# Kernel tuning notes

Hardware: AMD Instinct MI355X
Metric: run time of the kernel (lower is better)

Reference implementation:

```python
import jax, jax.numpy as jnp
import numpy as np

B, S, D_IN, D_OUT, RANK = 4, 2048, 4096, 4096, 16
ALPHA = 16
SCALING = ALPHA / RANK  # 1.0


def setup_inputs() -> dict:
    key = jax.random.key(0)
    k_x, k_q, k_b, k_a, k_bb = jax.random.split(key, 5)
    x = jax.random.normal(k_x, (B, S, D_IN), dtype=jnp.float32)
    # int4 symmetric quantized weight values in [-8, 7], stored as int32
    qweight = jax.random.randint(k_q, (D_OUT, D_IN), -8, 8, dtype=jnp.int32)
    # per-tensor scale (abs_max / 7 in the original); a plausible small value
    scales = jnp.array([0.01], dtype=jnp.float32)
    bias = jax.random.normal(k_b, (D_OUT,), dtype=jnp.float32) * 0.02
    # LoRA params (acting as "trained" values; original inits A kaiming, B zeros)
    lora_A = jax.random.normal(k_a, (D_IN, RANK), dtype=jnp.float32) * (1.0 / np.sqrt(D_IN))
    lora_B = jax.random.normal(k_bb, (RANK, D_OUT), dtype=jnp.float32) * 0.01
    return {"x": x, "qweight": qweight, "scales": scales, "bias": bias,
            "lora_A": lora_A, "lora_B": lora_B}


def reference(x, qweight, scales, bias, lora_A, lora_B):
    # dequantize: int4 values * scalar scale -> fp32 weight [D_OUT, D_IN]
    w = qweight.astype(jnp.float32) * scales[0]
    # F.linear(x, w, bias): x @ w.T + bias
    out = jnp.einsum('bsd,od->bso', x, w) + bias
    # LoRA low-rank path: (x @ A) @ B * scaling (dropout=0 -> identity)
    lora_out = (x @ lora_A) @ lora_B
    return out + lora_out * SCALING
```

## Files before the change

kernel.cpp:

```cpp
#include <hip/hip_runtime.h>
#include <stdint.h>
#include <math.h>


static constexpr int Mdim = 8192;
static constexpr int Ndim = 4096;
static constexpr int Kdim = 4096;

typedef __bf16 bf16x8 __attribute__((ext_vector_type(8)));
typedef float f32x4 __attribute__((ext_vector_type(4)));
typedef int   i32x4 __attribute__((ext_vector_type(4)));

__device__ __forceinline__ void async_copy16(const void* gptr, void* lptr) {
    auto g = (const __attribute__((address_space(1))) unsigned char*)(uintptr_t)gptr;
    auto l = (__attribute__((address_space(3))) unsigned char*)(uintptr_t)lptr;
    __builtin_amdgcn_global_load_lds(g, l, 16, 0, 0);
}

#define ASM_VMCNT4 asm volatile("s_waitcnt vmcnt(4)" ::: "memory")
#define ASM_VMCNT0 asm volatile("s_waitcnt vmcnt(0)" ::: "memory")

static constexpr int BLK_W = Ndim * Kdim / (256 * 16);
static constexpr int BLK_X = Mdim;
static constexpr int BLK_BT = Ndim / 256;

__global__ void __launch_bounds__(256) prep_kernel(
        const float* __restrict__ x,
        const int* __restrict__ qw,
        const float* __restrict__ lA,
        const float* __restrict__ lB,
        int8_t* __restrict__ x_i8,
        int8_t* __restrict__ w_i8,
        int8_t* __restrict__ a_i8t,
        __bf16* __restrict__ Blbt,
        float* __restrict__ row_scale,
        float* __restrict__ a_scale_g,
        float* __restrict__ xabf) {
    __shared__ float red[8];
    int b = blockIdx.x;
    const int tid = threadIdx.x;

    if (b == 0) {
        float am = 0.f;
        const float4* ap = (const float4*)lA + tid * 64;
        for (int i = 0; i < 64; ++i) {
            float4 v = ap[i];
            am = fmaxf(am, fmaxf(fmaxf(fabsf(v.x), fabsf(v.y)),
                                 fmaxf(fabsf(v.z), fabsf(v.w))));
        }
        for (int off = 32; off; off >>= 1) am = fmaxf(am, __shfl_xor(am, off));
        if ((tid & 63) == 0) red[tid >> 6] = am;
        __syncthreads();
        if (tid == 0) {
            float m = fmaxf(fmaxf(red[0], red[1]), fmaxf(red[2], red[3]));
            red[4] = m;
            a_scale_g[0] = m > 0.f ? m / 127.f : 0.f;
        }
        __syncthreads();
        float amax = red[4];
        float inv = amax > 0.f ? 127.f / amax : 0.f;
        int k0 = tid * 16;
#pragma unroll
        for (int r = 0; r < 16; ++r) {
            int8_t o[16];
#pragma unroll
            for (int kk = 0; kk < 16; ++kk) {
                float v = lA[(size_t)(k0 + kk) * 16 + r];
                o[kk] = (int8_t)(int)rintf(v * inv);
            }
            *(i32x4*)(a_i8t + (size_t)r * Kdim + k0) = *(i32x4*)o;
        }
        return;
    }
    b -= 1;

    if (b < BLK_W) {
        size_t idx = ((size_t)b * 256 + tid) * 16;
        const int4* q = (const int4*)(qw + idx);
        int4 q0 = q[0], q1 = q[1], q2 = q[2], q3 = q[3];
        int8_t o[16] = {(int8_t)q0.x, (int8_t)q0.y, (int8_t)q0.z, (int8_t)q0.w,
                        (int8_t)q1.x, (int8_t)q1.y, (int8_t)q1.z, (int8_t)q1.w,
                        (int8_t)q2.x, (int8_t)q2.y, (int8_t)q2.z, (int8_t)q2.w,
                        (int8_t)q3.x, (int8_t)q3.y, (int8_t)q3.z, (int8_t)q3.w};
        *(i32x4*)(w_i8 + idx) = *(i32x4*)o;
        return;
    }
    b -= BLK_W;

    if (b < BLK_X) {
        const int row = b;
        const float4* xp = (const float4*)(x + (size_t)row * Kdim) + tid * 4;
        float4 v0 = xp[0], v1 = xp[1], v2 = xp[2], v3 = xp[3];
        float am = 0.f;
        am = fmaxf(am, fmaxf(fmaxf(fabsf(v0.x), fabsf(v0.y)), fmaxf(fabsf(v0.z), fabsf(v0.w))));
        am = fmaxf(am, fmaxf(fmaxf(fabsf(v1.x), fabsf(v1.y)), fmaxf(fabsf(v1.z), fabsf(v1.w))));
        am = fmaxf(am, fmaxf(fmaxf(fabsf(v2.x), fabsf(v2.y)), fmaxf(fabsf(v2.z), fabsf(v2.w))));
        am = fmaxf(am, fmaxf(fmaxf(fabsf(v3.x), fabsf(v3.y)), fmaxf(fabsf(v3.z), fabsf(v3.w))));
        for (int off = 32; off; off >>= 1) am = fmaxf(am, __shfl_xor(am, off));
        if ((tid & 63) == 0) red[tid >> 6] = am;
        __syncthreads();
        if (tid == 0) {
            float m = fmaxf(fmaxf(red[0], red[1]), fmaxf(red[2], red[3]));
            red[4] = m;
            row_scale[row] = m > 0.f ? m / 127.f : 0.f;
        }
        __syncthreads();
        float amax = red[4];
        float inv = amax > 0.f ? 127.f / amax : 0.f;
        float vv[16] = {v0.x, v0.y, v0.z, v0.w, v1.x, v1.y, v1.z, v1.w,
                        v2.x, v2.y, v2.z, v2.w, v3.x, v3.y, v3.z, v3.w};
        int8_t o[16];
#pragma unroll
        for (int i = 0; i < 16; ++i) o[i] = (int8_t)(int)rintf(vv[i] * inv);
        *(i32x4*)(x_i8 + (size_t)row * Kdim + tid * 16) = *(i32x4*)o;
        return;
    }
    b -= BLK_X;

    {
        int c = b * 256 + tid;
        __bf16 tmp[16];
#pragma unroll
        for (int r = 0; r < 16; ++r) tmp[r] = (__bf16)lB[(size_t)r * Ndim + c];
        *(bf16x8*)(Blbt + (size_t)c * 16) = *(bf16x8*)tmp;
        *(bf16x8*)(Blbt + (size_t)c * 16 + 8) = *(bf16x8*)(tmp + 8);
        f32x4 z = {0.f, 0.f, 0.f, 0.f};
        f32x4* zp = (f32x4*)(xabf + (size_t)(b * 256 + tid) * 32);
#pragma unroll
        for (int i = 0; i < 8; ++i) zp[i] = z;
    }
}

__global__ void __launch_bounds__(256) xa_kernel(
        const int8_t* __restrict__ x_i8,
        const int8_t* __restrict__ a_i8t,
        const float* __restrict__ row_scale,
        const float* __restrict__ a_scale_g,
        float* __restrict__ xabf) {
    __shared__ __align__(16) char sX[2][4096];
    __shared__ __align__(16) char sAq[2][1024];
    const int tid = threadIdx.x, wave = tid >> 6, lane = tid & 63;
    const int quad = lane >> 4, l16 = lane & 15;
    const int bm = blockIdx.x >> 2;
    const int kc = blockIdx.x & 3;
    const int kbeg = kc * (Kdim / 4);

    const size_t xoff = (size_t)(bm * 64 + (tid & 63)) * Kdim + (tid >> 6) * 16;
    const size_t aoff = (size_t)(tid & 15) * Kdim + (tid >> 4) * 16;

    i32x4 acc = {0, 0, 0, 0};
    async_copy16(x_i8 + xoff + kbeg, sX[0] + tid * 16);
    if (tid < 64) async_copy16(a_i8t + aoff + kbeg, sAq[0] + tid * 16);
    __syncthreads();
    int cur = 0;
    const int rdA = (quad * 64 + wave * 16 + l16) * 16;
    const int rdB = (quad * 16 + l16) * 16;
#pragma unroll 1
    for (int t = 0; t < 16; ++t) {
        if (t < 15) {
            async_copy16(x_i8 + xoff + kbeg + (t + 1) * 64, sX[cur ^ 1] + tid * 16);
            if (tid < 64)
                async_copy16(a_i8t + aoff + kbeg + (t + 1) * 64, sAq[cur ^ 1] + tid * 16);
        }
        i32x4 af = *(const i32x4*)(sX[cur] + rdA);
        i32x4 bf = *(const i32x4*)(sAq[cur] + rdB);
        acc = __builtin_amdgcn_mfma_i32_16x16x64_i8(af, bf, acc, 0, 0, 0);
        __syncthreads();
        cur ^= 1;
    }
    const float asc = a_scale_g[0];
    const int rl = wave * 16 + quad * 4;
#pragma unroll
    for (int r = 0; r < 4; ++r) {
        int grow = bm * 64 + rl + r;
        float v = (float)acc[r] * row_scale[grow] * asc;
        atomicAdd(xabf + (size_t)grow * 16 + l16, v);
    }
}

__global__ void __launch_bounds__(256) gemm_kernel(
        const int8_t* __restrict__ Xq,
        const int8_t* __restrict__ Wq,
        const float* __restrict__ scales,
        const float* __restrict__ bias,
        const float* __restrict__ row_scale,
        const float* __restrict__ xabf,
        const __bf16* __restrict__ Blbt,
        float* __restrict__ out) {
    __shared__ __align__(16) char smem[32768];

    const int tid = threadIdx.x, wave = tid >> 6, lane = tid & 63;
    const int wm = wave >> 1, wn = wave & 1;
    const int quad = lane >> 4, l16 = lane & 15;

    const int bid = blockIdx.y * gridDim.x + blockIdx.x;
    const int xcd = bid & 7;
    const int local = bid >> 3;
    const int bm = (xcd >> 1) * 16 + (local >> 4);
    const int bn = (xcd & 1) * 16 + (local & 15);

    const int srow = tid & 127;
    const int sq = tid >> 7;
    const size_t a_off0 = (size_t)(bm * 128 + srow) * Kdim + sq * 16;
    const size_t a_off1 = a_off0 + 32;
    const size_t b_off0 = (size_t)(bn * 128 + srow) * Kdim + sq * 16;
    const size_t b_off1 = b_off0 + 32;
    const int dst0 = tid * 16, dst1 = 4096 + tid * 16;

    const int aoffL = quad * 2048 + (wm * 64 + l16) * 16;
    const int boffL = quad * 2048 + (wn * 64 + l16) * 16;

    i32x4 acc[4][4];
#pragma unroll
    for (int i = 0; i < 4; ++i)
#pragma unroll
        for (int j = 0; j < 4; ++j) acc[i][j] = i32x4{0, 0, 0, 0};

    char* const sA0 = smem;
    char* const sB0 = smem + 8192;
    char* const sA1 = smem + 16384;
    char* const sB1 = smem + 24576;

    auto stage = [&](int k0, char* PA, char* PB) {
        async_copy16(Xq + a_off0 + k0, PA + dst0);
        async_copy16(Xq + a_off1 + k0, PA + dst1);
        async_copy16(Wq + b_off0 + k0, PB + dst0);
        async_copy16(Wq + b_off1 + k0, PB + dst1);
    };
    auto compute = [&](const char* PA, const char* PB) {
        i32x4 aF[4], bF[4];
#pragma unroll
        for (int i = 0; i < 4; ++i) aF[i] = *(const i32x4*)(PA + aoffL + i * 256);
#pragma unroll
        for (int j = 0; j < 4; ++j) bF[j] = *(const i32x4*)(PB + boffL + j * 256);
        __builtin_amdgcn_s_setprio(1);
#pragma unroll
        for (int i = 0; i < 4; ++i)
#pragma unroll
            for (int j = 0; j < 4; ++j)
                acc[i][j] = __builtin_amdgcn_mfma_i32_16x16x64_i8(aF[i], bF[j], acc[i][j], 0, 0, 0);
        __builtin_amdgcn_s_setprio(0);
    };

    stage(0, sA0, sB0);
#pragma unroll 1
    for (int t = 0; t < 31; ++t) {
        const int k = t * 128;
        stage(k + 64, sA1, sB1);
        ASM_VMCNT4;
        __builtin_amdgcn_s_barrier();
        compute(sA0, sB0);
        __builtin_amdgcn_s_barrier();
        stage(k + 128, sA0, sB0);
        ASM_VMCNT4;
        __builtin_amdgcn_s_barrier();
        compute(sA1, sB1);
        __builtin_amdgcn_s_barrier();
    }
    stage(63 * 64, sA1, sB1);
    ASM_VMCNT4;
    __builtin_amdgcn_s_barrier();
    compute(sA0, sB0);
    __builtin_amdgcn_s_barrier();
    ASM_VMCNT0;
    __builtin_amdgcn_s_barrier();
    compute(sA1, sB1);

    const float wsc = scales[0];
    float bj4[4];
#pragma unroll
    for (int j = 0; j < 4; ++j) bj4[j] = bias[bn * 128 + wn * 64 + j * 16 + l16];

    __syncthreads();
    async_copy16((const char*)xabf + (size_t)bm * 128 * 64 + tid * 16, smem + tid * 16);
    async_copy16((const char*)xabf + (size_t)bm * 128 * 64 + 4096 + tid * 16,
                 smem + 4096 + tid * 16);
    async_copy16((const char*)(Blbt + (size_t)bn * 128 * 16) + tid * 16,
                 smem + 8192 + tid * 16);
    if (tid < 32)
        async_copy16((const char*)(row_scale + bm * 128) + tid * 16,
                     smem + 12288 + tid * 16);
    __syncthreads();

    const float*  sXAf = (const float*)smem;
    const __bf16* sBL  = (const __bf16*)(smem + 8192);
    const float*  sRS  = (const float*)(smem + 12288);

    bf16x8 zf;
#pragma unroll
    for (int k = 0; k < 8; ++k) zf[k] = (__bf16)0.f;

    bf16x8 aF2[4], bF2[4];
#pragma unroll
    for (int i = 0; i < 4; ++i) {
        if (quad < 2) {
            const float* p = sXAf + (wm * 64 + i * 16 + l16) * 16 + quad * 8;
            f32x4 u0 = *(const f32x4*)p;
            f32x4 u1 = *(const f32x4*)(p + 4);
            bf16x8 t;
            t[0] = (__bf16)u0[0]; t[1] = (__bf16)u0[1];
            t[2] = (__bf16)u0[2]; t[3] = (__bf16)u0[3];
            t[4] = (__bf16)u1[0]; t[5] = (__bf16)u1[1];
            t[6] = (__bf16)u1[2]; t[7] = (__bf16)u1[3];
            aF2[i] = t;
        } else {
            aF2[i] = zf;
        }
    }
#pragma unroll
    for (int j = 0; j < 4; ++j) {
        if (quad < 2) bF2[j] = *(const bf16x8*)(sBL + (wn * 64 + j * 16 + l16) * 16 + quad * 8);
        else          bF2[j] = zf;
    }

    f32x4 lacc[4][4];
#pragma unroll
    for (int j = 0; j < 4; ++j)
#pragma unroll
        for (int i = 0; i < 4; ++i)
            lacc[i][j] = f32x4{bj4[j], bj4[j], bj4[j], bj4[j]};

#pragma unroll
    for (int i = 0; i < 4; ++i)
#pragma unroll
        for (int j = 0; j < 4; ++j)
            lacc[i][j] = __builtin_amdgcn_mfma_f32_16x16x32_bf16(aF2[i], bF2[j], lacc[i][j], 0, 0, 0);

    const int col0 = bn * 128 + wn * 64 + l16;
    const int rl0 = wm * 64 + quad * 4;
#pragma unroll
    for (int j = 0; j < 4; ++j) {
        const int col = col0 + j * 16;
#pragma unroll
        for (int i = 0; i < 4; ++i) {
            const int lr = rl0 + i * 16;
#pragma unroll
            for (int r = 0; r < 4; ++r) {
                float sx = sRS[lr + r] * wsc;
                out[(size_t)(bm * 128 + lr + r) * Ndim + col] =
                    (float)acc[i][j][r] * sx + lacc[i][j][r];
            }
        }
    }
}

extern "C" void kernel_launch(void* const* d_in, const int* in_sizes, int n_in,
                              void* d_out, int out_size, void* d_ws, size_t ws_size,
                              hipStream_t stream) {
    const float* x      = (const float*)d_in[0];
    const int*   qw     = (const int*)d_in[1];
    const float* scales = (const float*)d_in[2];
    const float* bias   = (const float*)d_in[3];
    const float* lA     = (const float*)d_in[4];
    const float* lB     = (const float*)d_in[5];
    float* out = (float*)d_out;

    char* ws = (char*)d_ws;
    int8_t* x_i8     = (int8_t*)ws;
    int8_t* w_i8     = (int8_t*)(ws + 33554432);
    int8_t* a_i8t    = (int8_t*)(ws + 50331648);
    float*  xabf     = (float*)(ws + 50397184);
    __bf16* Blbt     = (__bf16*)(ws + 50921472);
    float*  row_scale = (float*)(ws + 51052544);
    float*  a_scale_g = (float*)(ws + 51085312);

    const int prep_blocks = 1 + BLK_W + BLK_X + BLK_BT;
    prep_kernel<<<prep_blocks, 256, 0, stream>>>(
        x, qw, lA, lB, x_i8, w_i8, a_i8t, Blbt, row_scale, a_scale_g, xabf);
    xa_kernel<<<512, 256, 0, stream>>>(x_i8, a_i8t, row_scale, a_scale_g, xabf);
    dim3 grid(Ndim / 128, Mdim / 128);
    gemm_kernel<<<grid, 256, 0, stream>>>(x_i8, w_i8, scales, bias, row_scale,
                                          xabf, Blbt, out);
}
```

Baseline: 554.2 us.

## Enlarge int8 GEMM tile to 256x256 with 512 threads and triple buffering

The int8 GEMM moves from 128x128 tiles with 4 waves and double buffering to 256x256 tiles with 8 waves, each wave owning a 128x64 sub-tile, plus a three-stage LDS ring (96 KB) that keeps two loads in flight. Block-to-tile mapping is reworked so each XCD takes a contiguous band of rows. The larger tile is meant to roughly halve global and LDS traffic per MFMA, and the deeper pipeline is meant to hide load latency better. In exchange it uses more accumulator registers and much more LDS, which lowers occupancy, and the grid shrinks to 512 blocks, which can cause tail imbalance across CUs.

```diff
diff --git a/kernel.cpp b/kernel.cpp
--- a/kernel.cpp
+++ b/kernel.cpp
@@ -17,6 +17,7 @@
     __builtin_amdgcn_global_load_lds(g, l, 16, 0, 0);
 }
 
+#define ASM_VMCNT8 asm volatile("s_waitcnt vmcnt(8)" ::: "memory")
 #define ASM_VMCNT4 asm volatile("s_waitcnt vmcnt(4)" ::: "memory")
 #define ASM_VMCNT0 asm volatile("s_waitcnt vmcnt(0)" ::: "memory")
 
@@ -178,7 +179,7 @@
     }
 }
 
-__global__ void __launch_bounds__(256) gemm_kernel(
+__global__ void __launch_bounds__(512, 2) gemm_kernel(
         const int8_t* __restrict__ Xq,
         const int8_t* __restrict__ Wq,
         const float* __restrict__ scales,
@@ -187,114 +188,124 @@
         const float* __restrict__ xabf,
         const __bf16* __restrict__ Blbt,
         float* __restrict__ out) {
-    __shared__ __align__(16) char smem[32768];
-
-    const int tid = threadIdx.x, wave = tid >> 6, lane = tid & 63;
-    const int wm = wave >> 1, wn = wave & 1;
+    __shared__ __align__(16) char smem[98304];
+
+    const int tid = threadIdx.x;
+    const int wave = tid >> 6, lane = tid & 63;
+    const int wm = wave >> 2, wn = wave & 3;
     const int quad = lane >> 4, l16 = lane & 15;
 
     const int bid = blockIdx.y * gridDim.x + blockIdx.x;
     const int xcd = bid & 7;
     const int local = bid >> 3;
-    const int bm = (xcd >> 1) * 16 + (local >> 4);
-    const int bn = (xcd & 1) * 16 + (local & 15);
-
-    const int srow = tid & 127;
-    const int sq = tid >> 7;
-    const size_t a_off0 = (size_t)(bm * 128 + srow) * Kdim + sq * 16;
-    const size_t a_off1 = a_off0 + 32;
-    const size_t b_off0 = (size_t)(bn * 128 + srow) * Kdim + sq * 16;
-    const size_t b_off1 = b_off0 + 32;
-    const int dst0 = tid * 16, dst1 = 4096 + tid * 16;
-
-    const int aoffL = quad * 2048 + (wm * 64 + l16) * 16;
-    const int boffL = quad * 2048 + (wn * 64 + l16) * 16;
-
-    i32x4 acc[4][4];
-#pragma unroll
-    for (int i = 0; i < 4; ++i)
+    const int bm = xcd * 4 + (local >> 4);
+    const int bn = local & 15;
+
+    const size_t a_base0 = (size_t)(bm * 256 + (tid & 255)) * Kdim + (tid >> 8) * 16;
+    const size_t a_base1 = a_base0 + 32;
+    const size_t b_base0 = (size_t)(bn * 256 + (tid & 255)) * Kdim + (tid >> 8) * 16;
+    const size_t b_base1 = b_base0 + 32;
+    const int dst0 = tid * 16, dst1 = 8192 + tid * 16;
+
+    const int qplane = quad * 4096;
+    const int arowb = (wm * 128 + l16) * 16;
+    const int browb = (wn * 64 + l16) * 16;
+
+    i32x4 acc[8][4];
+#pragma unroll
+    for (int i = 0; i < 8; ++i)
 #pragma unroll
         for (int j = 0; j < 4; ++j) acc[i][j] = i32x4{0, 0, 0, 0};
 
-    char* const sA0 = smem;
-    char* const sB0 = smem + 8192;
-    char* const sA1 = smem + 16384;
-    char* const sB1 = smem + 24576;
-
-    auto stage = [&](int k0, char* PA, char* PB) {
-        async_copy16(Xq + a_off0 + k0, PA + dst0);
-        async_copy16(Xq + a_off1 + k0, PA + dst1);
-        async_copy16(Wq + b_off0 + k0, PB + dst0);
-        async_copy16(Wq + b_off1 + k0, PB + dst1);
+    char* const R0 = smem;
+    char* const R1 = smem + 32768;
+    char* const R2 = smem + 65536;
+
+    auto stage = [&](int k0, char* buf) {
+        char* PB = buf + 16384;
+        async_copy16(Xq + a_base0 + k0, buf + dst0);
+        async_copy16(Xq + a_base1 + k0, buf + dst1);
+        async_copy16(Wq + b_base0 + k0, PB + dst0);
+        async_copy16(Wq + b_base1 + k0, PB + dst1);
     };
-    auto compute = [&](const char* PA, const char* PB) {
-        i32x4 aF[4], bF[4];
-#pragma unroll
-        for (int i = 0; i < 4; ++i) aF[i] = *(const i32x4*)(PA + aoffL + i * 256);
-#pragma unroll
-        for (int j = 0; j < 4; ++j) bF[j] = *(const i32x4*)(PB + boffL + j * 256);
-        __builtin_amdgcn_s_setprio(1);
-#pragma unroll
-        for (int i = 0; i < 4; ++i)
-#pragma unroll
-            for (int j = 0; j < 4; ++j)
-                acc[i][j] = __builtin_amdgcn_mfma_i32_16x16x64_i8(aF[i], bF[j], acc[i][j], 0, 0, 0);
-        __builtin_amdgcn_s_setprio(0);
+    auto compute = [&](const char* buf) {
+        const char* PB = buf + 16384;
+#pragma unroll
+        for (int qd = 0; qd < 4; ++qd) {
+            const int i0 = (qd & 1) * 4, j0 = (qd >> 1) * 2;
+            i32x4 aF[4], bF[2];
+#pragma unroll
+            for (int ii = 0; ii < 4; ++ii)
+                aF[ii] = *(const i32x4*)(buf + qplane + arowb + (i0 + ii) * 256);
+#pragma unroll
+            for (int jj = 0; jj < 2; ++jj)
+                bF[jj] = *(const i32x4*)(PB + qplane + browb + (j0 + jj) * 256);
+            __builtin_amdgcn_s_setprio(1);
+#pragma unroll
+            for (int ii = 0; ii < 4; ++ii)
+#pragma unroll
+                for (int jj = 0; jj < 2; ++jj)
+                    acc[i0 + ii][j0 + jj] = __builtin_amdgcn_mfma_i32_16x16x64_i8(
+                        aF[ii], bF[jj], acc[i0 + ii][j0 + jj], 0, 0, 0);
+            __builtin_amdgcn_s_setprio(0);
+        }
     };
-
-    stage(0, sA0, sB0);
+    auto step_full = [&](int k, char* bc, char* bs, int ks) {
+        stage(ks, bs);
+        ASM_VMCNT8;
+        __builtin_amdgcn_s_barrier();
+        compute(bc);
+        __builtin_amdgcn_s_barrier();
+    };
+
+    stage(0, R0);
+    stage(64, R1);
 #pragma unroll 1
-    for (int t = 0; t < 31; ++t) {
-        const int k = t * 128;
-        stage(k + 64, sA1, sB1);
-        ASM_VMCNT4;
-        __builtin_amdgcn_s_barrier();
-        compute(sA0, sB0);
-        __builtin_amdgcn_s_barrier();
-        stage(k + 128, sA0, sB0);
-        ASM_VMCNT4;
-        __builtin_amdgcn_s_barrier();
-        compute(sA1, sB1);
-        __builtin_amdgcn_s_barrier();
-    }
-    stage(63 * 64, sA1, sB1);
+    for (int u = 0; u < 20; ++u) {
+        const int k = u * 192;
+        step_full(k,       R0, R2, k + 128);
+        step_full(k + 64,  R1, R0, k + 192);
+        step_full(k + 128, R2, R1, k + 256);
+    }
+    step_full(60 * 64, R0, R2, 62 * 64);
+    step_full(61 * 64, R1, R0, 63 * 64);
     ASM_VMCNT4;
     __builtin_amdgcn_s_barrier();
-    compute(sA0, sB0);
+    compute(R2);
     __builtin_amdgcn_s_barrier();
     ASM_VMCNT0;
     __builtin_amdgcn_s_barrier();
-    compute(sA1, sB1);
+    compute(R0);
 
     const float wsc = scales[0];
     float bj4[4];
 #pragma unroll
-    for (int j = 0; j < 4; ++j) bj4[j] = bias[bn * 128 + wn * 64 + j * 16 + l16];
+    for (int j = 0; j < 4; ++j) bj4[j] = bias[bn * 256 + wn * 64 + j * 16 + l16];
 
     __syncthreads();
-    async_copy16((const char*)xabf + (size_t)bm * 128 * 64 + tid * 16, smem + tid * 16);
-    async_copy16((const char*)xabf + (size_t)bm * 128 * 64 + 4096 + tid * 16,
-                 smem + 4096 + tid * 16);
-    async_copy16((const char*)(Blbt + (size_t)bn * 128 * 16) + tid * 16,
+    async_copy16((const char*)xabf + (size_t)bm * 256 * 64 + tid * 16, smem + tid * 16);
+    async_copy16((const char*)xabf + (size_t)bm * 256 * 64 + 8192 + tid * 16,
                  smem + 8192 + tid * 16);
-    if (tid < 32)
-        async_copy16((const char*)(row_scale + bm * 128) + tid * 16,
-                     smem + 12288 + tid * 16);
+    async_copy16((const char*)(Blbt + (size_t)bn * 256 * 16) + tid * 16,
+                 smem + 16384 + tid * 16);
+    if (tid < 64)
+        async_copy16((const char*)(row_scale + bm * 256) + tid * 16,
+                     smem + 24576 + tid * 16);
     __syncthreads();
 
     const float*  sXAf = (const float*)smem;
-    const __bf16* sBL  = (const __bf16*)(smem + 8192);
-    const float*  sRS  = (const float*)(smem + 12288);
+    const __bf16* sBL  = (const __bf16*)(smem + 16384);
+    const float*  sRS  = (const float*)(smem + 24576);
 
     bf16x8 zf;
 #pragma unroll
     for (int k = 0; k < 8; ++k) zf[k] = (__bf16)0.f;
 
-    bf16x8 aF2[4], bF2[4];
-#pragma unroll
-    for (int i = 0; i < 4; ++i) {
+    bf16x8 aF2[8], bF2[4];
+#pragma unroll
+    for (int i = 0; i < 8; ++i) {
         if (quad < 2) {
-            const float* p = sXAf + (wm * 64 + i * 16 + l16) * 16 + quad * 8;
+            const float* p = sXAf + (wm * 128 + i * 16 + l16) * 16 + quad * 8;
             f32x4 u0 = *(const f32x4*)p;
             f32x4 u1 = *(const f32x4*)(p + 4);
             bf16x8 t;
@@ -313,35 +324,25 @@
         else          bF2[j] = zf;
     }
 
-    f32x4 lacc[4][4];
-#pragma unroll
-    for (int j = 0; j < 4; ++j)
-#pragma unroll
-        for (int i = 0; i < 4; ++i)
-            lacc[i][j] = f32x4{bj4[j], bj4[j], bj4[j], bj4[j]};
-
-#pragma unroll
-    for (int i = 0; i < 4; ++i)
-#pragma unroll
-        for (int j = 0; j < 4; ++j)
-            lacc[i][j] = __builtin_amdgcn_mfma_f32_16x16x32_bf16(aF2[i], bF2[j], lacc[i][j], 0, 0, 0);
-
-    const int col0 = bn * 128 + wn * 64 + l16;
-    const int rl0 = wm * 64 + quad * 4;
-#pragma unroll
-    for (int j = 0; j < 4; ++j) {
-        const int col = col0 + j * 16;
-#pragma unroll
-        for (int i = 0; i < 4; ++i) {
-            const int lr = rl0 + i * 16;
+    const int col0 = bn * 256 + wn * 64 + l16;
+    const int rbase = bm * 256 + wm * 128 + quad * 4;
+#pragma unroll
+    for (int i = 0; i < 8; ++i) {
+#pragma unroll
+        for (int j = 0; j < 4; ++j) {
+            f32x4 l = f32x4{bj4[j], bj4[j], bj4[j], bj4[j]};
+            l = __builtin_amdgcn_mfma_f32_16x16x32_bf16(aF2[i], bF2[j], l, 0, 0, 0);
+            const int col = col0 + j * 16;
+            const int lr = wm * 128 + i * 16 + quad * 4;
 #pragma unroll
             for (int r = 0; r < 4; ++r) {
                 float sx = sRS[lr + r] * wsc;
-                out[(size_t)(bm * 128 + lr + r) * Ndim + col] =
-                    (float)acc[i][j][r] * sx + lacc[i][j][r];
+                out[(size_t)(bm * 256 + lr + r) * Ndim + col] =
+                    (float)acc[i][j][r] * sx + l[r];
             }
         }
     }
+    (void)rbase;
 }
 
 extern "C" void kernel_launch(void* const* d_in, const int* in_sizes, int n_in,
@@ -368,7 +369,7 @@
     prep_kernel<<<prep_blocks, 256, 0, stream>>>(
         x, qw, lA, lB, x_i8, w_i8, a_i8t, Blbt, row_scale, a_scale_g, xabf);
     xa_kernel<<<512, 256, 0, stream>>>(x_i8, a_i8t, row_scale, a_scale_g, xabf);
-    dim3 grid(Ndim / 128, Mdim / 128);
-    gemm_kernel<<<grid, 256, 0, stream>>>(x_i8, w_i8, scales, bias, row_scale,
+    dim3 grid(Ndim / 256, Mdim / 256);
+    gemm_kernel<<<grid, 512, 0, stream>>>(x_i8, w_i8, scales, bias, row_scale,
                                           xabf, Blbt, out);
 }
```

Result: faster. 487.0 us (-12.1%).
